# Optimization experiments

Hardware: AMD Instinct MI355X
Metric: run time of the kernel (lower is better)

The kernel has to match this reference:

```python
import jax, jax.numpy as jnp
import numpy as np
from jax import lax

STRIDE0, WS, PS, K = 4, 9, 3, 10
LVLS = 4
_MEAN = jnp.array([0.485, 0.456, 0.406], jnp.float32).reshape(1, 1, 3, 1, 1)
_STD = jnp.array([0.229, 0.224, 0.225], jnp.float32).reshape(1, 1, 3, 1, 1)


def _conv7(x, w, b):
    y = lax.conv_general_dilated(x, w, (1, 1), ((3, 3), (3, 3)),
                                 dimension_numbers=('NCHW', 'OIHW', 'NCHW'))
    return y + b[None, :, None, None]


def _basic(x, l, Ws):
    w1, b1, w2, b2, w3, b3, w4, b4, w5, b5 = [W[l] for W in Ws]
    x = jax.nn.relu(_conv7(x, w1, b1))
    x = jax.nn.relu(_conv7(x, w2, b2))
    x = jax.nn.relu(_conv7(x, w3, b3))
    x = jax.nn.relu(_conv7(x, w4, b4))
    return _conv7(x, w5, b5)


def _pool2(x):
    N, C, H, W = x.shape
    return x.reshape(N, C, H // 2, 2, W // 2, 2).mean(axis=(3, 5))


def _bsample(img, y, x):
    # img [N,C,H,W]; y,x [N,Hq,Wq] absolute float coords; border-clamped bilinear
    N, C, H, W = img.shape
    y = jnp.clip(y, 0., H - 1.)
    x = jnp.clip(x, 0., W - 1.)
    y0 = jnp.floor(y)
    x0 = jnp.floor(x)
    wy = (y - y0)[:, None]
    wx = (x - x0)[:, None]
    y0i = y0.astype(jnp.int32)
    x0i = x0.astype(jnp.int32)
    y1i = jnp.minimum(y0i + 1, H - 1)
    x1i = jnp.minimum(x0i + 1, W - 1)
    imgf = img.reshape(N, C, H * W)

    def g(yi, xi):
        idx = (yi * W + xi).reshape(N, 1, -1)
        return jnp.take_along_axis(imgf, idx, 2).reshape(N, C, *y.shape[1:])

    return (g(y0i, x0i) * (1 - wy) * (1 - wx) + g(y0i, x1i) * (1 - wy) * wx
            + g(y1i, x0i) * wy * (1 - wx) + g(y1i, x1i) * wy * wx)


def _spynet(ref, supp, Ws):
    # coarse-to-fine residual flow estimation (SpyNet)
    refs, sups = [ref], [supp]
    for _ in range(LVLS - 1):
        refs.append(_pool2(refs[-1]))
        sups.append(_pool2(sups[-1]))
    N = ref.shape[0]
    Hc, Wc = refs[-1].shape[2:]
    flow = jnp.zeros((N, 2, Hc, Wc), ref.dtype)
    for l in range(LVLS - 1, -1, -1):
        Hl, Wl = refs[l].shape[2:]
        if l < LVLS - 1:
            flow = 2. * jax.image.resize(flow, (N, 2, Hl, Wl), 'bilinear')
        gy, gx = jnp.meshgrid(jnp.arange(Hl, dtype=flow.dtype),
                              jnp.arange(Wl, dtype=flow.dtype), indexing='ij')
        warped = _bsample(sups[l], gy[None] + flow[:, 1], gx[None] + flow[:, 0])
        flow = flow + _basic(jnp.concatenate([refs[l], warped, flow], 1), l, Ws)
    return flow


def _bgather(vidf, ry, rx, H, W, C):
    # vidf [B,T,C,H*W]; ry,rx [B,T,*rest] float coords pre-clipped to valid range
    B, T = vidf.shape[:2]
    rest = ry.shape[2:]
    y0 = jnp.floor(ry)
    x0 = jnp.floor(rx)
    wy = (ry - y0)[:, :, None]
    wx = (rx - x0)[:, :, None]
    y0i = y0.astype(jnp.int32)
    x0i = x0.astype(jnp.int32)
    y1i = jnp.minimum(y0i + 1, H - 1)
    x1i = jnp.minimum(x0i + 1, W - 1)

    def g(yi, xi):
        idx = (yi * W + xi).reshape(B, T, 1, -1)
        return jnp.take_along_axis(vidf, idx, 3).reshape(B, T, C, *rest)

    return (g(y0i, x0i) * (1 - wy) * (1 - wx) + g(y0i, x1i) * (1 - wy) * wx
            + g(y1i, x0i) * wy * (1 - wx) + g(y1i, x1i) * wy * wx)


def _forward(vid, Ws):
    B, T, C, H, W = vid.shape
    # --- SpyNet flows between consecutive frames ---
    nv = (vid - _MEAN) / _STD
    ref = nv[:, :-1].reshape(B * (T - 1), C, H, W)
    sup = nv[:, 1:].reshape(B * (T - 1), C, H, W)
    fflow = _spynet(ref, sup, Ws).reshape(B, T - 1, 2, H, W)
    bflow = _spynet(sup, ref, Ws).reshape(B, T - 1, 2, H, W)
    z = jnp.zeros((B, 1, 2, H, W), vid.dtype)
    fflow = jnp.concatenate([fflow, z], 1)  # flow t -> t+1 (last frame zero)
    bflow = jnp.concatenate([z, bflow], 1)  # flow t -> t-1 (first frame zero)

    # --- flow-guided windowed non-local search (wt=1, skip_self=False) ---
    nH, nW = H // STRIDE0, W // STRIDE0
    qh = jnp.arange(nH) * STRIDE0
    qw = jnp.arange(nW) * STRIDE0
    fg = fflow[:, :, :, qh][:, :, :, :, qw]  # [B,T,2,nH,nW] flow at query grid
    bg = bflow[:, :, :, qh][:, :, :, :, qw]
    dp = jnp.arange(PS) - PS // 2
    offs = jnp.arange(WS) - WS // 2
    oh = jnp.repeat(offs, WS).astype(vid.dtype)  # [WS*WS] row offsets
    ow = jnp.tile(offs, WS).astype(vid.dtype)    # [WS*WS] col offsets

    # query patches (integer grid, clamped)
    yqi = jnp.clip(qh[:, None] + dp[None], 0, H - 1)
    xqi = jnp.clip(qw[:, None] + dp[None], 0, W - 1)
    qp = vid[:, :, :, yqi][..., xqi]           # [B,T,C,nH,PS,nW,PS]
    qp = qp.transpose(0, 1, 2, 3, 5, 4, 6)     # [B,T,C,nH,nW,PS,PS]
    qpe = qp[:, :, :, :, :, None, None]        # broadcast over (ws,ws)

    vidf = vid.reshape(B, T, C, H * W)
    qhf = qh.astype(vid.dtype)
    qwf = qw.astype(vid.dtype)
    offsf = offs.astype(vid.dtype)
    dpf = dp.astype(vid.dtype)
    zf = jnp.zeros((B, T, nH, nW), vid.dtype)

    flows_k = []
    for dt, fh, fw in ((0, zf, zf), (1, fg[:, :, 1], fg[:, :, 0]),
                       (-1, bg[:, :, 1], bg[:, :, 0])):
        tid = jnp.clip(jnp.arange(T) + dt, 0, T - 1)
        frf = vidf[:, tid]  # target frames, edge-clamped in time
        ry = (qhf[None, None, :, None, None, None] + fh[:, :, :, :, None, None]
              + offsf[None, None, None, None, :, None]
              + dpf[None, None, None, None, None, :])  # [B,T,nH,nW,WS,PS]
        rx = (qwf[None, None, None, :, None, None] + fw[:, :, :, :, None, None]
              + offsf[None, None, None, None, :, None]
              + dpf[None, None, None, None, None, :])
        ry = jnp.clip(ry, 0., H - 1.)
        rx = jnp.clip(rx, 0., W - 1.)
        RY = jnp.broadcast_to(ry[:, :, :, :, :, None, :, None],
                              (B, T, nH, nW, WS, WS, PS, PS))
        RX = jnp.broadcast_to(rx[:, :, :, :, None, :, None, :],
                              (B, T, nH, nW, WS, WS, PS, PS))
        cand = _bgather(frf, RY, RX, H, W, C)  # [B,T,C,nH,nW,WS,WS,PS,PS]
        dist = ((qpe - cand) ** 2).sum(axis=(2, -2, -1))  # [B,T,nH,nW,WS,WS]
        dist = dist.reshape(B, T, nH, nW, WS * WS)
        _, idx = lax.top_k(-dist, K)  # [B,T,nH,nW,K]
        dh = fh[..., None] + oh[idx]
        dw = fw[..., None] + ow[idx]
        dts = jnp.full_like(dh, float(dt))
        flows_k.append(jnp.stack([dts, dh, dw], axis=-1))
    return jnp.concatenate(flows_k, axis=-2)  # [B,T,nH,nW,3*K,3]


def setup_inputs():
    key = jax.random.key(0)
    ks = jax.random.split(key, 6)
    B, T, C, H, W = 1, 4, 3, 192, 192
    L = LVLS

    def w(k, shape):
        return jax.random.normal(k, shape, jnp.float32) * 0.02

    return {
        "vid": jax.random.normal(ks[0], (B, T, C, H, W), jnp.float32),
        "w1": w(ks[1], (L, 32, 8, 7, 7)), "b1": jnp.zeros((L, 32), jnp.float32),
        "w2": w(ks[2], (L, 64, 32, 7, 7)), "b2": jnp.zeros((L, 64), jnp.float32),
        "w3": w(ks[3], (L, 32, 64, 7, 7)), "b3": jnp.zeros((L, 32), jnp.float32),
        "w4": w(ks[4], (L, 16, 32, 7, 7)), "b4": jnp.zeros((L, 16), jnp.float32),
        "w5": w(ks[5], (L, 2, 16, 7, 7)), "b5": jnp.zeros((L, 2), jnp.float32),
    }


def reference(vid, w1, b1, w2, b2, w3, b3, w4, b4, w5, b5):
    return _forward(vid, (w1, b1, w2, b2, w3, b3, w4, b4, w5, b5))
```

## Files before the change

### kernel.cpp

```cpp
#include <hip/hip_runtime.h>
#include <cstdint>

#define H0 192
#define W0 192
#define TT 4
#define NBATCH 6

__global__ void k_normalize(const float* __restrict__ vid, float* __restrict__ nv) {
    int idx = blockIdx.x * 256 + threadIdx.x;
    const int total = TT * 3 * H0 * W0;
    if (idx >= total) return;
    int c = (idx / (H0 * W0)) % 3;
    float m = (c == 0) ? 0.485f : (c == 1) ? 0.456f : 0.406f;
    float s = (c == 0) ? 0.229f : (c == 1) ? 0.224f : 0.225f;
    nv[idx] = (vid[idx] - m) / s;
}

__global__ void k_pool(const float* __restrict__ in, float* __restrict__ out,
                       int NC, int Ho, int Wo) {
    int idx = blockIdx.x * 256 + threadIdx.x;
    int total = NC * Ho * Wo;
    if (idx >= total) return;
    int x = idx % Wo;
    int y = (idx / Wo) % Ho;
    int nc = idx / (Wo * Ho);
    const float* p = in + ((size_t)nc * (Ho * 2) + y * 2) * (size_t)(Wo * 2) + x * 2;
    int Wi = Wo * 2;
    out[idx] = (p[0] + p[1] + p[Wi] + p[Wi + 1]) * 0.25f;
}

__global__ void k_upsample2x(const float* __restrict__ in, float* __restrict__ out,
                             int NC, int Hi, int Wi) {
    int Ho = Hi * 2, Wo = Wi * 2;
    int idx = blockIdx.x * 256 + threadIdx.x;
    int total = NC * Ho * Wo;
    if (idx >= total) return;
    int x = idx % Wo;
    int y = (idx / Wo) % Ho;
    int nc = idx / (Wo * Ho);
    int ky = y >> 1, kx = x >> 1;
    int y0, y1, x0, x1;
    float wy0, wy1, wx0, wx1;
    if ((y & 1) == 0) {
        if (ky == 0) { y0 = 0; y1 = 0; wy0 = 1.f; wy1 = 0.f; }
        else { y0 = ky - 1; y1 = ky; wy0 = 0.25f; wy1 = 0.75f; }
    } else {
        if (ky == Hi - 1) { y0 = ky; y1 = ky; wy0 = 1.f; wy1 = 0.f; }
        else { y0 = ky; y1 = ky + 1; wy0 = 0.75f; wy1 = 0.25f; }
    }
    if ((x & 1) == 0) {
        if (kx == 0) { x0 = 0; x1 = 0; wx0 = 1.f; wx1 = 0.f; }
        else { x0 = kx - 1; x1 = kx; wx0 = 0.25f; wx1 = 0.75f; }
    } else {
        if (kx == Wi - 1) { x0 = kx; x1 = kx; wx0 = 1.f; wx1 = 0.f; }
        else { x0 = kx; x1 = kx + 1; wx0 = 0.75f; wx1 = 0.25f; }
    }
    const float* base = in + (size_t)nc * Hi * Wi;
    float v = wy0 * (wx0 * base[(size_t)y0 * Wi + x0] + wx1 * base[(size_t)y0 * Wi + x1])
            + wy1 * (wx0 * base[(size_t)y1 * Wi + x0] + wx1 * base[(size_t)y1 * Wi + x1]);
    out[idx] = 2.0f * v;
}

__global__ void k_build_in8(const float* __restrict__ pyr, const float* __restrict__ flow,
                            float* __restrict__ in8, int H, int W) {
    int idx = blockIdx.x * 256 + threadIdx.x;
    int total = NBATCH * H * W;
    if (idx >= total) return;
    int x = idx % W;
    int y = (idx / W) % H;
    int n = idx / (W * H);
    int ref_f = (n < 3) ? n : n - 2;
    int sup_f = (n < 3) ? n + 1 : n - 3;
    size_t hw = (size_t)H * W;
    float fx = flow[((size_t)n * 2 + 0) * hw + (size_t)y * W + x];
    float fy = flow[((size_t)n * 2 + 1) * hw + (size_t)y * W + x];
    float ry = (float)y + fy;
    float rx = (float)x + fx;
    ry = fminf(fmaxf(ry, 0.f), (float)(H - 1));
    rx = fminf(fmaxf(rx, 0.f), (float)(W - 1));
    float y0f = floorf(ry), x0f = floorf(rx);
    float wy = ry - y0f, wx = rx - x0f;
    int y0 = (int)y0f, x0 = (int)x0f;
    int y1 = min(y0 + 1, H - 1), x1 = min(x0 + 1, W - 1);
    const float* sup = pyr + (size_t)sup_f * 3 * hw;
    const float* ref = pyr + (size_t)ref_f * 3 * hw;
    float* o = in8 + (size_t)n * 8 * hw + (size_t)y * W + x;
    #pragma unroll
    for (int c = 0; c < 3; c++) {
        const float* sc = sup + (size_t)c * hw;
        float g00 = sc[(size_t)y0 * W + x0], g01 = sc[(size_t)y0 * W + x1];
        float g10 = sc[(size_t)y1 * W + x0], g11 = sc[(size_t)y1 * W + x1];
        float v = g00 * (1.f - wy) * (1.f - wx) + g01 * (1.f - wy) * wx
                + g10 * wy * (1.f - wx) + g11 * wy * wx;
        o[(size_t)(3 + c) * hw] = v;
        o[(size_t)c * hw] = ref[(size_t)c * hw + (size_t)y * W + x];
    }
    o[6 * hw] = fx;
    o[7 * hw] = fy;
}


template<int NR, int ISZ>
__device__ __forceinline__ void conv_iload(const float* __restrict__ ip, float* sreg,
        int tid, int by, int bx, int H, int W) {
    #pragma unroll
    for (int k = 0; k < NR; k++) {
        int tpos = tid + k * 256;
        int ly = tpos / 39;
        int lx = tpos - ly * 39;
        int gy = by + ly - 3, gx = bx + lx - 3;
        bool ok = (tpos < ISZ) && (lx < 38) && ((unsigned)gy < (unsigned)H) && ((unsigned)gx < (unsigned)W);
        sreg[k] = ok ? ip[gy * W + gx] : 0.f;
    }
}

template<int OCB, int NWR, int NWELEM>
__device__ __forceinline__ void conv_wload(const float* __restrict__ wt, float* wreg,
        int tid, int oc0, int IC, int cbase) {
    #pragma unroll
    for (int k = 0; k < NWR; k++) {
        int tpos = tid + k * 256;
        int oc = tpos / 392;
        int rem = tpos - oc * 392;
        int icc = rem / 49;
        int kk = rem - icc * 49;
        wreg[k] = (tpos < NWELEM) ? wt[((size_t)(oc0 + oc) * IC + (cbase + icc)) * 49 + kk] : 0.f;
    }
}

template<int OCB, int RPT, bool RELU, bool ACC>
__global__ __launch_bounds__(256) void k_conv(
        const float* __restrict__ in, const float* __restrict__ wt,
        const float* __restrict__ bias, float* __restrict__ out,
        int IC, int OC, int H, int W, int ntx, int nty, int nocg) {
    constexpr int TH = RPT * 32;
    constexpr int IROWS = TH + 6;
    constexpr int ISZ = IROWS * 39;
    constexpr int NR = (ISZ + 255) / 256;
    constexpr int WROW = 52;
    constexpr int NWELEM = OCB * 8 * 49;
    constexpr int NWR = (NWELEM + 255) / 256;
    __shared__ float smi[2 * ISZ];
    __shared__ float smw[8 * OCB * WROW];

    int nwg = gridDim.x, wg = blockIdx.x;
    int q = nwg >> 3, r = nwg & 7;
    int xcd = wg & 7, pos = wg >> 3;
    int logical = ((xcd < r) ? xcd * (q + 1) : r * (q + 1) + (xcd - r) * q) + pos;
    int ocg = logical % nocg; int t2 = logical / nocg;
    int tx = t2 % ntx; t2 /= ntx;
    int ty = t2 % nty; int n = t2 / nty;
    int oc0 = ocg * OCB;
    int bx = tx * 32, by = ty * TH;
    int tid = threadIdx.x;
    int tq = tid & 7, trow = tid >> 3;
    int hw = H * W;

    float acc[OCB][RPT][4];
    #pragma unroll
    for (int o = 0; o < OCB; o++)
        #pragma unroll
        for (int rr = 0; rr < RPT; rr++)
            #pragma unroll
            for (int p = 0; p < 4; p++) acc[o][rr][p] = 0.f;

    const float* ip0 = in + (size_t)n * IC * hw;
    float sreg[NR];
    float wreg[NWR];

    conv_wload<OCB, NWR, NWELEM>(wt, wreg, tid, oc0, IC, 0);
    conv_iload<NR, ISZ>(ip0, sreg, tid, by, bx, H, W);
    #pragma unroll
    for (int k = 0; k < NR; k++) {
        int tpos = tid + k * 256;
        if (tpos < ISZ) smi[tpos] = sreg[k];
    }
    if (IC > 1) conv_iload<NR, ISZ>(ip0 + hw, sreg, tid, by, bx, H, W);

    for (int ic = 0; ic < IC; ++ic) {
        int cur = ic & 1;
        if ((ic & 7) == 0) {
            #pragma unroll
            for (int k = 0; k < NWR; k++) {
                int tpos = tid + k * 256;
                int oc = tpos / 392;
                int rem = tpos - oc * 392;
                int icc = rem / 49;
                int kk = rem - icc * 49;
                if (tpos < NWELEM) smw[(icc * OCB + oc) * WROW + kk] = wreg[k];
            }
            __syncthreads();
            if (ic + 8 < IC) conv_wload<OCB, NWR, NWELEM>(wt, wreg, tid, oc0, IC, ic + 8);
        }
        if (ic + 1 < IC) {
            #pragma unroll
            for (int k = 0; k < NR; k++) {
                int tpos = tid + k * 256;
                if (tpos < ISZ) smi[(cur ^ 1) * ISZ + tpos] = sreg[k];
            }
            if (ic + 2 < IC)
                conv_iload<NR, ISZ>(ip0 + (size_t)(ic + 2) * hw, sreg, tid, by, bx, H, W);
        }
        int icc = ic & 7;
        const float* smc = smi + cur * ISZ + trow * 39 + tq * 4;
        #pragma unroll
        for (int ky = 0; ky < 7; ++ky) {
            float xin[RPT][10];
            #pragma unroll
            for (int rr = 0; rr < RPT; rr++)
                #pragma unroll
                for (int off = 0; off < 10; off++)
                    xin[rr][off] = smc[(rr * 32 + ky) * 39 + off];
            #pragma unroll
            for (int oc = 0; oc < OCB; ++oc) {
                const float* wrow = smw + (icc * OCB + oc) * WROW + ky * 7;
                #pragma unroll
                for (int kx = 0; kx < 7; ++kx) {
                    float wv = wrow[kx];
                    #pragma unroll
                    for (int rr = 0; rr < RPT; rr++)
                        #pragma unroll
                        for (int p = 0; p < 4; p++)
                            acc[oc][rr][p] = fmaf(xin[rr][kx + p], wv, acc[oc][rr][p]);
                }
            }
        }
        __syncthreads();
    }

    int ox0 = bx + tq * 4;
    #pragma unroll
    for (int rr = 0; rr < RPT; rr++) {
        int oy = by + trow + rr * 32;
        if (oy < H) {
            #pragma unroll
            for (int oc = 0; oc < OCB; ++oc) {
                float bv = bias[oc0 + oc];
                float v[4];
                #pragma unroll
                for (int p = 0; p < 4; p++) {
                    v[p] = acc[oc][rr][p] + bv;
                    if (RELU) v[p] = fmaxf(v[p], 0.f);
                }
                float* op = out + ((size_t)n * OC + oc0 + oc) * hw + (size_t)oy * W + ox0;
                if (ox0 + 3 < W) {
                    if (ACC) {
                        float4 o4 = *(const float4*)op;
                        o4.x += v[0]; o4.y += v[1]; o4.z += v[2]; o4.w += v[3];
                        *(float4*)op = o4;
                    } else {
                        *(float4*)op = make_float4(v[0], v[1], v[2], v[3]);
                    }
                } else {
                    #pragma unroll
                    for (int p = 0; p < 4; p++)
                        if (ox0 + p < W) { if (ACC) op[p] += v[p]; else op[p] = v[p]; }
                }
            }
        }
    }
}

__global__ __launch_bounds__(64) void k_match(
        const float* __restrict__ vid, const float* __restrict__ flow,
        float* __restrict__ out) {
    int q = blockIdx.x;
    int j = q % 48; q /= 48;
    int i = q % 48; q /= 48;
    int t = q % 4;
    int dtIdx = q / 4;
    int lane = threadIdx.x;

    float fh = 0.f, fw = 0.f, dtf = 0.f;
    int tid = t;
    if (dtIdx == 1) {
        if (t < 3) {
            size_t base = (((size_t)t * 2) * 192 + i * 4) * 192 + j * 4;
            fw = flow[base];
            fh = flow[base + (size_t)192 * 192];
        }
        tid = min(t + 1, 3);
        dtf = 1.f;
    } else if (dtIdx == 2) {
        if (t > 0) {
            size_t base = (((size_t)(t + 2) * 2) * 192 + i * 4) * 192 + j * 4;
            fw = flow[base];
            fh = flow[base + (size_t)192 * 192];
        }
        tid = max(t - 1, 0);
        dtf = -1.f;
    }

    __shared__ int sy0[27], sy1[27], sx0[27], sx1[27];
    __shared__ float sfy[27], sfx[27], qp[27];
    if (lane < 27) {
        int wq = lane / 3, p = lane % 3;
        float ry = (((float)(i * 4) + fh) + (float)(wq - 4)) + (float)(p - 1);
        ry = fminf(fmaxf(ry, 0.f), 191.f);
        float y0f = floorf(ry);
        int y0 = (int)y0f;
        sy0[lane] = y0; sy1[lane] = min(y0 + 1, 191); sfy[lane] = ry - y0f;
        float rx = (((float)(j * 4) + fw) + (float)(wq - 4)) + (float)(p - 1);
        rx = fminf(fmaxf(rx, 0.f), 191.f);
        float x0f = floorf(rx);
        int x0 = (int)x0f;
        sx0[lane] = x0; sx1[lane] = min(x0 + 1, 191); sfx[lane] = rx - x0f;
        int c = lane / 9, pp = lane % 9, py = pp / 3, px = pp % 3;
        int yy = min(max(i * 4 + py - 1, 0), 191);
        int xx = min(max(j * 4 + px - 1, 0), 191);
        qp[lane] = vid[(((size_t)t * 3 + c) * 192 + yy) * 192 + xx];
    }
    __syncthreads();

    const float* frame = vid + (size_t)tid * 3 * 192 * 192;
    float dist[2];
    int widx[2];
    #pragma unroll
    for (int r = 0; r < 2; r++) {
        int w = lane + 64 * r;
        if (w < 81) {
            int wy = w / 9, wx = w % 9;
            float dsum = 0.f;
            for (int c = 0; c < 3; c++) {
                const float* fc = frame + (size_t)c * 36864;
                #pragma unroll
                for (int py = 0; py < 3; py++) {
                    int ye = wy * 3 + py;
                    int y0 = sy0[ye], y1 = sy1[ye];
                    float fy = sfy[ye];
                    const float* r0 = fc + (size_t)y0 * 192;
                    const float* r1 = fc + (size_t)y1 * 192;
                    #pragma unroll
                    for (int px = 0; px < 3; px++) {
                        int xe = wx * 3 + px;
                        int x0 = sx0[xe], x1 = sx1[xe];
                        float fx = sfx[xe];
                        float g00 = r0[x0], g01 = r0[x1], g10 = r1[x0], g11 = r1[x1];
                        float cand = g00 * (1.f - fy) * (1.f - fx) + g01 * (1.f - fy) * fx
                                   + g10 * fy * (1.f - fx) + g11 * fy * fx;
                        float diff = qp[(c * 3 + py) * 3 + px] - cand;
                        dsum = fmaf(diff, diff, dsum);
                    }
                }
            }
            dist[r] = dsum; widx[r] = w;
        } else {
            dist[r] = __builtin_inff(); widx[r] = 1000;
        }
    }

    for (int k = 0; k < 10; k++) {
        float d = dist[0]; int wi = widx[0];
        if (dist[1] < d || (dist[1] == d && widx[1] < wi)) { d = dist[1]; wi = widx[1]; }
        #pragma unroll
        for (int off = 32; off >= 1; off >>= 1) {
            float od = __shfl_xor(d, off);
            int ow = __shfl_xor(wi, off);
            if (od < d || (od == d && ow < wi)) { d = od; wi = ow; }
        }
        if (lane == 0) {
            size_t ob = ((((size_t)t * 48 + i) * 48 + j) * 30 + dtIdx * 10 + k) * 3;
            out[ob + 0] = dtf;
            out[ob + 1] = fh + (float)(wi / 9 - 4);
            out[ob + 2] = fw + (float)(wi % 9 - 4);
        }
        if (widx[0] == wi) dist[0] = __builtin_inff();
        if (widx[1] == wi) dist[1] = __builtin_inff();
    }
}

extern "C" void kernel_launch(void* const* d_in, const int* in_sizes, int n_in,
                              void* d_out, int out_size, void* d_ws, size_t ws_size,
                              hipStream_t stream) {
    const float* vid = (const float*)d_in[0];
    const float* w1 = (const float*)d_in[1];  const float* b1 = (const float*)d_in[2];
    const float* w2 = (const float*)d_in[3];  const float* b2 = (const float*)d_in[4];
    const float* w3 = (const float*)d_in[5];  const float* b3 = (const float*)d_in[6];
    const float* w4 = (const float*)d_in[7];  const float* b4 = (const float*)d_in[8];
    const float* w5 = (const float*)d_in[9];  const float* b5 = (const float*)d_in[10];
    float* out = (float*)d_out;
    float* ws = (float*)d_ws;

    float* nv    = ws;
    float* pyr1  = nv    + 442368;
    float* pyr2  = pyr1  + 110592;
    float* pyr3  = pyr2  + 27648;
    float* flowA = pyr3  + 6912;
    float* flowB = flowA + 442368;
    float* in8   = flowB + 442368;
    float* bufA  = in8   + 1769472;
    float* bufB  = bufA  + 7077888;

    k_normalize<<<(442368 + 255) / 256, 256, 0, stream>>>(vid, nv);
    k_pool<<<(110592 + 255) / 256, 256, 0, stream>>>(nv, pyr1, 12, 96, 96);
    k_pool<<<(27648 + 255) / 256, 256, 0, stream>>>(pyr1, pyr2, 12, 48, 48);
    k_pool<<<(6912 + 255) / 256, 256, 0, stream>>>(pyr2, pyr3, 12, 24, 24);

    const float* pyrs[4] = {nv, pyr1, pyr2, pyr3};

    float* cur = flowA;
    float* oth = flowB;
    hipMemsetAsync(cur, 0, (size_t)NBATCH * 2 * 24 * 24 * 4, stream);
    for (int l = 3; l >= 0; --l) {
        int H = H0 >> l, W = W0 >> l;
        if (l < 3) {
            k_upsample2x<<<((12 * H * W) + 255) / 256, 256, 0, stream>>>(cur, oth, 12, H / 2, W / 2);
            float* tsw = cur; cur = oth; oth = tsw;
        }
        k_build_in8<<<((NBATCH * H * W) + 255) / 256, 256, 0, stream>>>(pyrs[l], cur, in8, H, W);

        const float* W1 = w1 + (size_t)l * 32 * 8 * 49;  const float* B1 = b1 + l * 32;
        const float* W2 = w2 + (size_t)l * 64 * 32 * 49; const float* B2 = b2 + l * 64;
        const float* W3 = w3 + (size_t)l * 32 * 64 * 49; const float* B3 = b3 + l * 32;
        const float* W4 = w4 + (size_t)l * 16 * 32 * 49; const float* B4 = b4 + l * 16;
        const float* W5 = w5 + (size_t)l * 2 * 16 * 49;  const float* B5 = b5 + l * 2;

        if (l == 0) {
            k_conv<4, 2, true,  false><<<6 * 3 * 8 * 6, 256, 0, stream>>>(in8,  W1, B1, bufA, 8,  32, H, W, 6, 3, 8);
            k_conv<8, 2, true,  false><<<6 * 3 * 8 * 6, 256, 0, stream>>>(bufA, W2, B2, bufB, 32, 64, H, W, 6, 3, 8);
            k_conv<4, 2, true,  false><<<6 * 3 * 8 * 6, 256, 0, stream>>>(bufB, W3, B3, bufA, 64, 32, H, W, 6, 3, 8);
            k_conv<2, 2, true,  false><<<6 * 3 * 8 * 6, 256, 0, stream>>>(bufA, W4, B4, bufB, 32, 16, H, W, 6, 3, 8);
            k_conv<1, 1, false, true ><<<6 * 6 * 2 * 6, 256, 0, stream>>>(bufB, W5, B5, cur,  16, 2,  H, W, 6, 6, 2);
        } else {
            int nt = (H + 31) / 32;
            k_conv<4, 1, true,  false><<<nt * nt * 8 * 6, 256, 0, stream>>>(in8,  W1, B1, bufA, 8,  32, H, W, nt, nt, 8);
            k_conv<8, 1, true,  false><<<nt * nt * 8 * 6, 256, 0, stream>>>(bufA, W2, B2, bufB, 32, 64, H, W, nt, nt, 8);
            k_conv<4, 1, true,  false><<<nt * nt * 8 * 6, 256, 0, stream>>>(bufB, W3, B3, bufA, 64, 32, H, W, nt, nt, 8);
            k_conv<2, 1, true,  false><<<nt * nt * 8 * 6, 256, 0, stream>>>(bufA, W4, B4, bufB, 32, 16, H, W, nt, nt, 8);
            k_conv<1, 1, false, true ><<<nt * nt * 2 * 6, 256, 0, stream>>>(bufB, W5, B5, cur,  16, 2,  H, W, nt, nt, 2);
        }
    }

    k_match<<<27648, 64, 0, stream>>>(vid, cur, out);
}
```

Before: 3.472 ms.

## Pad conv shared tiles for vector LDS reads and unify 32-row tiling

Input tiles in shared memory now use a padded 44-float row stride and weights an 8-float padded row, so each thread reads its 10 inputs and 7 weights with float4/float2 loads instead of scalar loads. The two-rows-per-thread variant used at full resolution is dropped in favor of one 32x32 tile per block everywhere, with launch bounds asking for 4 blocks per CU. The last two layers use larger output-channel blocks. This cuts LDS instruction count and raises occupancy, but loses the input-row reuse of the two-row variant and launches more blocks at level 0.

```diff
diff --git a/kernel.cpp b/kernel.cpp
--- a/kernel.cpp
+++ b/kernel.cpp
@@ -100,23 +100,40 @@
 }
 
 
-template<int NR, int ISZ>
+#define IW 38
+#define ISTR 44
+#define NI (IW * IW)
+#define ISZ (IW * ISTR)
+#define NR 6
+
 __device__ __forceinline__ void conv_iload(const float* __restrict__ ip, float* sreg,
         int tid, int by, int bx, int H, int W) {
     #pragma unroll
     for (int k = 0; k < NR; k++) {
         int tpos = tid + k * 256;
-        int ly = tpos / 39;
-        int lx = tpos - ly * 39;
+        int ly = tpos / IW;
+        int lx = tpos - ly * IW;
         int gy = by + ly - 3, gx = bx + lx - 3;
-        bool ok = (tpos < ISZ) && (lx < 38) && ((unsigned)gy < (unsigned)H) && ((unsigned)gx < (unsigned)W);
+        bool ok = (tpos < NI) && ((unsigned)gy < (unsigned)H) && ((unsigned)gx < (unsigned)W);
         sreg[k] = ok ? ip[gy * W + gx] : 0.f;
     }
 }
 
-template<int OCB, int NWR, int NWELEM>
+__device__ __forceinline__ void conv_istore(float* __restrict__ dst, const float* sreg,
+        int tid) {
+    #pragma unroll
+    for (int k = 0; k < NR; k++) {
+        int tpos = tid + k * 256;
+        int ly = tpos / IW;
+        int lx = tpos - ly * IW;
+        if (tpos < NI) dst[ly * ISTR + lx] = sreg[k];
+    }
+}
+
+template<int OCB, int NWR>
 __device__ __forceinline__ void conv_wload(const float* __restrict__ wt, float* wreg,
         int tid, int oc0, int IC, int cbase) {
+    constexpr int NWELEM = OCB * 8 * 49;
     #pragma unroll
     for (int k = 0; k < NWR; k++) {
         int tpos = tid + k * 256;
@@ -128,20 +145,15 @@
     }
 }
 
-template<int OCB, int RPT, bool RELU, bool ACC>
-__global__ __launch_bounds__(256) void k_conv(
+template<int OCB, bool RELU, bool ACC>
+__global__ __launch_bounds__(256, 4) void k_conv(
         const float* __restrict__ in, const float* __restrict__ wt,
         const float* __restrict__ bias, float* __restrict__ out,
         int IC, int OC, int H, int W, int ntx, int nty, int nocg) {
-    constexpr int TH = RPT * 32;
-    constexpr int IROWS = TH + 6;
-    constexpr int ISZ = IROWS * 39;
-    constexpr int NR = (ISZ + 255) / 256;
-    constexpr int WROW = 52;
     constexpr int NWELEM = OCB * 8 * 49;
     constexpr int NWR = (NWELEM + 255) / 256;
     __shared__ float smi[2 * ISZ];
-    __shared__ float smw[8 * OCB * WROW];
+    __shared__ float smw[8 * OCB * 7 * 8];
 
     int nwg = gridDim.x, wg = blockIdx.x;
     int q = nwg >> 3, r = nwg & 7;
@@ -151,31 +163,25 @@
     int tx = t2 % ntx; t2 /= ntx;
     int ty = t2 % nty; int n = t2 / nty;
     int oc0 = ocg * OCB;
-    int bx = tx * 32, by = ty * TH;
+    int bx = tx * 32, by = ty * 32;
     int tid = threadIdx.x;
     int tq = tid & 7, trow = tid >> 3;
     int hw = H * W;
 
-    float acc[OCB][RPT][4];
+    float acc[OCB][4];
     #pragma unroll
     for (int o = 0; o < OCB; o++)
         #pragma unroll
-        for (int rr = 0; rr < RPT; rr++)
-            #pragma unroll
-            for (int p = 0; p < 4; p++) acc[o][rr][p] = 0.f;
+        for (int p = 0; p < 4; p++) acc[o][p] = 0.f;
 
     const float* ip0 = in + (size_t)n * IC * hw;
     float sreg[NR];
     float wreg[NWR];
 
-    conv_wload<OCB, NWR, NWELEM>(wt, wreg, tid, oc0, IC, 0);
-    conv_iload<NR, ISZ>(ip0, sreg, tid, by, bx, H, W);
-    #pragma unroll
-    for (int k = 0; k < NR; k++) {
-        int tpos = tid + k * 256;
-        if (tpos < ISZ) smi[tpos] = sreg[k];
-    }
-    if (IC > 1) conv_iload<NR, ISZ>(ip0 + hw, sreg, tid, by, bx, H, W);
+    conv_wload<OCB, NWR>(wt, wreg, tid, oc0, IC, 0);
+    conv_iload(ip0, sreg, tid, by, bx, H, W);
+    conv_istore(smi, sreg, tid);
+    if (IC > 1) conv_iload(ip0 + hw, sreg, tid, by, bx, H, W);
 
     for (int ic = 0; ic < IC; ++ic) {
         int cur = ic & 1;
@@ -183,45 +189,41 @@
             #pragma unroll
             for (int k = 0; k < NWR; k++) {
                 int tpos = tid + k * 256;
-                int oc = tpos / 392;
-                int rem = tpos - oc * 392;
-                int icc = rem / 49;
-                int kk = rem - icc * 49;
-                if (tpos < NWELEM) smw[(icc * OCB + oc) * WROW + kk] = wreg[k];
+                if (tpos < NWELEM) {
+                    int oc = tpos / 392;
+                    int rem = tpos - oc * 392;
+                    int icc = rem / 49;
+                    int kk = rem - icc * 49;
+                    int ky = kk / 7, kx = kk - ky * 7;
+                    smw[((icc * OCB + oc) * 7 + ky) * 8 + kx] = wreg[k];
+                }
             }
             __syncthreads();
-            if (ic + 8 < IC) conv_wload<OCB, NWR, NWELEM>(wt, wreg, tid, oc0, IC, ic + 8);
+            if (ic + 8 < IC) conv_wload<OCB, NWR>(wt, wreg, tid, oc0, IC, ic + 8);
         }
         if (ic + 1 < IC) {
-            #pragma unroll
-            for (int k = 0; k < NR; k++) {
-                int tpos = tid + k * 256;
-                if (tpos < ISZ) smi[(cur ^ 1) * ISZ + tpos] = sreg[k];
-            }
+            conv_istore(smi + (cur ^ 1) * ISZ, sreg, tid);
             if (ic + 2 < IC)
-                conv_iload<NR, ISZ>(ip0 + (size_t)(ic + 2) * hw, sreg, tid, by, bx, H, W);
+                conv_iload(ip0 + (size_t)(ic + 2) * hw, sreg, tid, by, bx, H, W);
         }
         int icc = ic & 7;
-        const float* smc = smi + cur * ISZ + trow * 39 + tq * 4;
+        const float* smc = smi + cur * ISZ + trow * ISTR + tq * 4;
         #pragma unroll
         for (int ky = 0; ky < 7; ++ky) {
-            float xin[RPT][10];
-            #pragma unroll
-            for (int rr = 0; rr < RPT; rr++)
-                #pragma unroll
-                for (int off = 0; off < 10; off++)
-                    xin[rr][off] = smc[(rr * 32 + ky) * 39 + off];
+            float4 xa = *(const float4*)(smc + ky * ISTR);
+            float4 xb = *(const float4*)(smc + ky * ISTR + 4);
+            float2 xc = *(const float2*)(smc + ky * ISTR + 8);
+            float xin[10] = {xa.x, xa.y, xa.z, xa.w, xb.x, xb.y, xb.z, xb.w, xc.x, xc.y};
             #pragma unroll
             for (int oc = 0; oc < OCB; ++oc) {
-                const float* wrow = smw + (icc * OCB + oc) * WROW + ky * 7;
+                const float4* wp = (const float4*)(smw + ((icc * OCB + oc) * 7 + ky) * 8);
+                float4 wa = wp[0], wb = wp[1];
+                float wv[7] = {wa.x, wa.y, wa.z, wa.w, wb.x, wb.y, wb.z};
                 #pragma unroll
                 for (int kx = 0; kx < 7; ++kx) {
-                    float wv = wrow[kx];
                     #pragma unroll
-                    for (int rr = 0; rr < RPT; rr++)
-                        #pragma unroll
-                        for (int p = 0; p < 4; p++)
-                            acc[oc][rr][p] = fmaf(xin[rr][kx + p], wv, acc[oc][rr][p]);
+                    for (int p = 0; p < 4; p++)
+                        acc[oc][p] = fmaf(xin[kx + p], wv[kx], acc[oc][p]);
                 }
             }
         }
@@ -229,33 +231,30 @@
     }
 
     int ox0 = bx + tq * 4;
-    #pragma unroll
-    for (int rr = 0; rr < RPT; rr++) {
-        int oy = by + trow + rr * 32;
-        if (oy < H) {
+    int oy = by + trow;
+    if (oy < H) {
+        #pragma unroll
+        for (int oc = 0; oc < OCB; ++oc) {
+            float bv = bias[oc0 + oc];
+            float v[4];
             #pragma unroll
-            for (int oc = 0; oc < OCB; ++oc) {
-                float bv = bias[oc0 + oc];
-                float v[4];
+            for (int p = 0; p < 4; p++) {
+                v[p] = acc[oc][p] + bv;
+                if (RELU) v[p] = fmaxf(v[p], 0.f);
+            }
+            float* op = out + ((size_t)n * OC + oc0 + oc) * hw + (size_t)oy * W + ox0;
+            if (ox0 + 3 < W) {
+                if (ACC) {
+                    float4 o4 = *(const float4*)op;
+                    o4.x += v[0]; o4.y += v[1]; o4.z += v[2]; o4.w += v[3];
+                    *(float4*)op = o4;
+                } else {
+                    *(float4*)op = make_float4(v[0], v[1], v[2], v[3]);
+                }
+            } else {
                 #pragma unroll
-                for (int p = 0; p < 4; p++) {
-                    v[p] = acc[oc][rr][p] + bv;
-                    if (RELU) v[p] = fmaxf(v[p], 0.f);
-                }
-                float* op = out + ((size_t)n * OC + oc0 + oc) * hw + (size_t)oy * W + ox0;
-                if (ox0 + 3 < W) {
-                    if (ACC) {
-                        float4 o4 = *(const float4*)op;
-                        o4.x += v[0]; o4.y += v[1]; o4.z += v[2]; o4.w += v[3];
-                        *(float4*)op = o4;
-                    } else {
-                        *(float4*)op = make_float4(v[0], v[1], v[2], v[3]);
-                    }
-                } else {
-                    #pragma unroll
-                    for (int p = 0; p < 4; p++)
-                        if (ox0 + p < W) { if (ACC) op[p] += v[p]; else op[p] = v[p]; }
-                }
+                for (int p = 0; p < 4; p++)
+                    if (ox0 + p < W) { if (ACC) op[p] += v[p]; else op[p] = v[p]; }
             }
         }
     }
@@ -415,20 +414,13 @@
         const float* W4 = w4 + (size_t)l * 16 * 32 * 49; const float* B4 = b4 + l * 16;
         const float* W5 = w5 + (size_t)l * 2 * 16 * 49;  const float* B5 = b5 + l * 2;
 
-        if (l == 0) {
-            k_conv<4, 2, true,  false><<<6 * 3 * 8 * 6, 256, 0, stream>>>(in8,  W1, B1, bufA, 8,  32, H, W, 6, 3, 8);
-            k_conv<8, 2, true,  false><<<6 * 3 * 8 * 6, 256, 0, stream>>>(bufA, W2, B2, bufB, 32, 64, H, W, 6, 3, 8);
-            k_conv<4, 2, true,  false><<<6 * 3 * 8 * 6, 256, 0, stream>>>(bufB, W3, B3, bufA, 64, 32, H, W, 6, 3, 8);
-            k_conv<2, 2, true,  false><<<6 * 3 * 8 * 6, 256, 0, stream>>>(bufA, W4, B4, bufB, 32, 16, H, W, 6, 3, 8);
-            k_conv<1, 1, false, true ><<<6 * 6 * 2 * 6, 256, 0, stream>>>(bufB, W5, B5, cur,  16, 2,  H, W, 6, 6, 2);
-        } else {
-            int nt = (H + 31) / 32;
-            k_conv<4, 1, true,  false><<<nt * nt * 8 * 6, 256, 0, stream>>>(in8,  W1, B1, bufA, 8,  32, H, W, nt, nt, 8);
-            k_conv<8, 1, true,  false><<<nt * nt * 8 * 6, 256, 0, stream>>>(bufA, W2, B2, bufB, 32, 64, H, W, nt, nt, 8);
-            k_conv<4, 1, true,  false><<<nt * nt * 8 * 6, 256, 0, stream>>>(bufB, W3, B3, bufA, 64, 32, H, W, nt, nt, 8);
-            k_conv<2, 1, true,  false><<<nt * nt * 8 * 6, 256, 0, stream>>>(bufA, W4, B4, bufB, 32, 16, H, W, nt, nt, 8);
-            k_conv<1, 1, false, true ><<<nt * nt * 2 * 6, 256, 0, stream>>>(bufB, W5, B5, cur,  16, 2,  H, W, nt, nt, 2);
-        }
+        int nt = (H + 31) / 32;
+        int ntt = nt * nt;
+        k_conv<4, true,  false><<<ntt * 8 * 6, 256, 0, stream>>>(in8,  W1, B1, bufA, 8,  32, H, W, nt, nt, 8);
+        k_conv<8, true,  false><<<ntt * 8 * 6, 256, 0, stream>>>(bufA, W2, B2, bufB, 32, 64, H, W, nt, nt, 8);
+        k_conv<4, true,  false><<<ntt * 8 * 6, 256, 0, stream>>>(bufB, W3, B3, bufA, 64, 32, H, W, nt, nt, 8);
+        k_conv<4, true,  false><<<ntt * 4 * 6, 256, 0, stream>>>(bufA, W4, B4, bufB, 32, 16, H, W, nt, nt, 4);
+        k_conv<2, false, true ><<<ntt * 1 * 6, 256, 0, stream>>>(bufB, W5, B5, cur,  16, 2,  H, W, nt, nt, 1);
     }
 
     k_match<<<27648, 64, 0, stream>>>(vid, cur, out);
```

After: 5.360 ms. 54.4% more time.
